# Optimization experiments

Measured on AMD Instinct MI355X. Metric: run time of the kernel, lower is better.

## Reference

```python
import jax, jax.numpy as jnp
import numpy as np

N = 262144   # collocation points (512x512 grid equivalent)
H = 64       # MLP hidden width
PI = np.float32(np.pi)


def setup_inputs() -> dict:
    key = jax.random.key(0)
    ks = jax.random.split(key, 6)
    def glorot(k, shp):
        scale = np.float32(np.sqrt(2.0 / (shp[0] + shp[1])))
        return jax.random.normal(k, shp, jnp.float32) * scale
    return {
        "points": jax.random.uniform(ks[0], (N, 2), jnp.float32),  # (x, t) in [0,1]^2
        "W1": glorot(ks[1], (2, H)), "b1": jnp.zeros((H,), jnp.float32),
        "W2": glorot(ks[2], (H, H)), "b2": jnp.zeros((H,), jnp.float32),
        "W3": glorot(ks[3], (H, H)), "b3": jnp.zeros((H,), jnp.float32),
        "Wo": glorot(ks[4], (H, 1)), "bo": jnp.zeros((1,), jnp.float32),
    }


def _mlp(pt, W1, b1, W2, b2, W3, b3, Wo, bo):
    # pt: [2] -> scalar u(x, t)
    h = jnp.tanh(pt @ W1 + b1)
    h = jnp.tanh(h @ W2 + b2)
    h = jnp.tanh(h @ W3 + b3)
    return (h @ Wo + bo)[0]


def reference(points, W1, b1, W2, b2, W3, b3, Wo, bo):
    params = (W1, b1, W2, b2, W3, b3, Wo, bo)
    dt = points.dtype
    keep_t = jnp.array([0.0, 1.0], dt)   # points * [0,1]
    set_x1 = jnp.array([1.0, 0.0], dt)   # + [1,0] -> (1, t)

    def psi_fn(pt):
        x, t = pt[0], pt[1]
        pt1t = pt * keep_t + set_x1                    # boundary point (1, t)
        u = _mlp(pt, *params)                          # u(x, t)
        u_1t = _mlp(pt1t, *params)                     # u(1, t)
        u1t_x = jax.grad(lambda p: _mlp(p, *params))(pt1t)[0]  # du/dx at (1, t)
        return (2.0 * x * jnp.sin(PI * t)
                + (t * t - t) * (x * x - x) * (u - u_1t - u1t_x))

    def loss_point(pt):
        x, t = pt[0], pt[1]
        psi, g1 = jax.value_and_grad(psi_fn)(pt)       # g1 = (psi_x, psi_t)
        # TF's tape.gradient sums over components of dpsi_dxdt, so:
        # h = grad(psi_x + psi_t) = (psi_xx + psi_tx, psi_xt + psi_tt)
        h = jax.grad(lambda p: jnp.sum(jax.grad(psi_fn)(p)))(pt)
        s = jnp.sin(PI * t)
        res = (h[0] + h[1] + psi * g1[0]
               - s * (2.0 - PI * PI * x * x + 2.0 * x ** 3 * s))
        return jnp.abs(res)

    return jnp.mean(jax.vmap(loss_point)(points))
```

## Files before the change

kernel.cpp:

```cpp
#include <hip/hip_runtime.h>
#include <math.h>

typedef _Float16 half_t;
typedef half_t half8 __attribute__((ext_vector_type(8)));
typedef __fp16 fp16x2 __attribute__((ext_vector_type(2)));
typedef float f32x4 __attribute__((ext_vector_type(4)));
typedef float f32x2 __attribute__((ext_vector_type(2)));

#define PI_F 3.14159265358979323846f

__device__ __forceinline__ f32x2 splat2(float s) { return f32x2{s, s}; }
__device__ __forceinline__ f32x2 fma2(f32x2 a, f32x2 b, f32x2 c) {
    return __builtin_elementwise_fma(a, b, c);
}

__device__ __forceinline__ f32x2 ftanh2(f32x2 z) {
    const f32x2 m = z * splat2(2.8853900817779268f);
    f32x2 t;
    t[0] = exp2f(m[0]);
    t[1] = exp2f(m[1]);
    const f32x2 s = t + splat2(1.f);
    f32x2 r;
    r[0] = __builtin_amdgcn_rcpf(s[0]);
    r[1] = __builtin_amdgcn_rcpf(s[1]);
    return fma2(splat2(-2.f), r, splat2(1.f));
}

__global__ __launch_bounds__(256) void pinn_main(
    const float* __restrict__ pts,
    const float* __restrict__ W1, const float* __restrict__ b1,
    const float* __restrict__ b2, const float* __restrict__ b3,
    const half_t* __restrict__ wsH,
    float* __restrict__ partial)
{
    __shared__ __align__(16) half_t J[160 * 64];
    __shared__ float ubuf[7][16];

    const int tid = threadIdx.x;
    const int l   = tid & 63;
    const int w   = tid >> 6;
    const int q   = l >> 4;
    const int i   = l & 15;
    const int ja  = w * 16 + i;
    const int jb  = w * 16 + q * 4;

    const int rb0 = i * 64 + ((q ^ (i & 7)) << 3);
    const int rb1 = i * 64 + (((4 + q) ^ (i & 7)) << 3);
    const int wbase = i * 64 + ((((w * 2 + (q >> 1)) ^ (i & 7))) << 3) + (q & 1) * 4;

    const half8 w2a = *(const half8*)(wsH + ja * 64 + q * 8);
    const half8 w2b = *(const half8*)(wsH + ja * 64 + 32 + q * 8);
    const half8 w3a = *(const half8*)(wsH + 4096 + ja * 64 + q * 8);
    const half8 w3b = *(const half8*)(wsH + 4096 + ja * 64 + 32 + q * 8);

    const float4 w04 = *(const float4*)(W1 + jb);
    const float4 w14 = *(const float4*)(W1 + 64 + jb);
    const float4 b14 = *(const float4*)(b1 + jb);
    const float4 b24 = *(const float4*)(b2 + jb);
    const float4 b34 = *(const float4*)(b3 + jb);

    half8 wo0 = {0, 0, 0, 0, 0, 0, 0, 0};
    half8 wo1 = {0, 0, 0, 0, 0, 0, 0, 0};
    if (i == 0) {
        wo0 = *(const half8*)(wsH + 8192 + q * 8);
        wo1 = *(const half8*)(wsH + 8192 + 32 + q * 8);
    }

    auto stc = [&](int c, f32x2 v01, f32x2 v23) {
        uint2 d;
        d.x = __builtin_bit_cast(unsigned int,
                                 __builtin_amdgcn_cvt_pkrtz(v01[0], v01[1]));
        d.y = __builtin_bit_cast(unsigned int,
                                 __builtin_amdgcn_cvt_pkrtz(v23[0], v23[1]));
        *(uint2*)(&J[wbase + c * 1024]) = d;
    };

    const f32x2 w0a = {w04.x, w04.y}, w0b = {w04.z, w04.w};
    const f32x2 w1a = {w14.x, w14.y}, w1b = {w14.z, w14.w};
    const f32x2 bba = {b14.x, b14.y}, bbb = {b14.z, b14.w};

    float bsum = 0.f;

    #pragma unroll 1
    for (int pass = 0; pass < 2; ++pass) {
        const int pbase = blockIdx.x * 32 + pass * 16;

        const float2 xy = *(const float2*)(pts + 2 * (pbase + i));
        const float X = xy.x, T = xy.y;

        {
            const f32x2 wda = w0a + w1a, wdb = w0b + w1b;
            const f32x2 zva = fma2(splat2(X), w0a, fma2(splat2(T), w1a, bba));
            const f32x2 zvb = fma2(splat2(X), w0b, fma2(splat2(T), w1b, bbb));
            const f32x2 aa = ftanh2(zva), ab = ftanh2(zvb);
            const f32x2 d1a = splat2(1.f) - aa * aa, d1b = splat2(1.f) - ab * ab;
            const f32x2 d2a = splat2(-2.f) * aa * d1a, d2b = splat2(-2.f) * ab * d1b;
            stc(0, aa, ab);
            stc(1, d1a * w0a, d1b * w0b);
            stc(2, d1a * wda, d1b * wdb);
            stc(3, d2a * wda * wda, d2b * wdb * wdb);
        }
        {
            const f32x2 zva = fma2(splat2(T), w1a, bba + w0a);
            const f32x2 zvb = fma2(splat2(T), w1b, bbb + w0b);
            const f32x2 aa = ftanh2(zva), ab = ftanh2(zvb);
            const f32x2 e1a = splat2(1.f) - aa * aa, e1b = splat2(1.f) - ab * ab;
            const f32x2 e2a = splat2(-2.f) * aa * e1a, e2b = splat2(-2.f) * ab * e1b;
            const f32x2 e3a = splat2(-2.f) * (e1a * e1a + aa * e2a);
            const f32x2 e3b = splat2(-2.f) * (e1b * e1b + ab * e2b);
            stc(4, aa, ab);
            stc(5, e1a * w0a, e1b * w0b);
            stc(6, e1a * w1a, e1b * w1b);
            stc(7, e2a * w0a * w1a, e2b * w0b * w1b);
            stc(8, e2a * w1a * w1a, e2b * w1b * w1b);
            stc(9, e3a * w0a * w1a * w1a, e3b * w0b * w1b * w1b);
        }

        auto layer_step = [&](const half8 A0, const half8 A1, const float4 b4,
                              bool combine) {
            __syncthreads();
            const f32x4 zb = {b4.x, b4.y, b4.z, b4.w};
            const f32x4 z0 = {0.f, 0.f, 0.f, 0.f};
            f32x4 acc[10];
            #pragma unroll
            for (int c = 0; c < 10; ++c) {
                const half8 f0 = *(const half8*)(&J[rb0 + c * 1024]);
                const half8 f1 = *(const half8*)(&J[rb1 + c * 1024]);
                f32x4 z = (c == 0 || c == 4) ? zb : z0;
                z = __builtin_amdgcn_mfma_f32_16x16x32_f16(A0, f0, z, 0, 0, 0);
                z = __builtin_amdgcn_mfma_f32_16x16x32_f16(A1, f1, z, 0, 0, 0);
                acc[c] = z;
            }
            __syncthreads();

            {
                const f32x2 zva = {acc[0][0], acc[0][1]}, zvb = {acc[0][2], acc[0][3]};
                const f32x2 aa = ftanh2(zva), ab = ftanh2(zvb);
                const f32x2 d1a = splat2(1.f) - aa * aa, d1b = splat2(1.f) - ab * ab;
                const f32x2 d2a = splat2(-2.f) * aa * d1a, d2b = splat2(-2.f) * ab * d1b;
                const f32x2 zxa = {acc[1][0], acc[1][1]}, zxb = {acc[1][2], acc[1][3]};
                const f32x2 zda = {acc[2][0], acc[2][1]}, zdb = {acc[2][2], acc[2][3]};
                const f32x2 zdda = {acc[3][0], acc[3][1]}, zddb = {acc[3][2], acc[3][3]};
                stc(0, aa, ab);
                stc(1, d1a * zxa, d1b * zxb);
                stc(2, d1a * zda, d1b * zdb);
                stc(3, fma2(d2a * zda, zda, d1a * zdda),
                       fma2(d2b * zdb, zdb, d1b * zddb));
            }
            {
                const f32x2 zva = {acc[4][0], acc[4][1]}, zvb = {acc[4][2], acc[4][3]};
                const f32x2 aa = ftanh2(zva), ab = ftanh2(zvb);
                const f32x2 e1a = splat2(1.f) - aa * aa, e1b = splat2(1.f) - ab * ab;
                const f32x2 e2a = splat2(-2.f) * aa * e1a, e2b = splat2(-2.f) * ab * e1b;
                const f32x2 e3a = splat2(-2.f) * (e1a * e1a + aa * e2a);
                const f32x2 e3b = splat2(-2.f) * (e1b * e1b + ab * e2b);
                const f32x2 zxa  = {acc[5][0], acc[5][1]},  zxb  = {acc[5][2], acc[5][3]};
                const f32x2 zta  = {acc[6][0], acc[6][1]},  ztb  = {acc[6][2], acc[6][3]};
                const f32x2 zxta = {acc[7][0], acc[7][1]},  zxtb = {acc[7][2], acc[7][3]};
                const f32x2 ztta = {acc[8][0], acc[8][1]},  zttb = {acc[8][2], acc[8][3]};
                const f32x2 zxtta = {acc[9][0], acc[9][1]}, zxttb = {acc[9][2], acc[9][3]};
                if (combine) {
                    stc(4, aa + e1a * zxa, ab + e1b * zxb);
                    stc(5, fma2(e2a * zxa, zta, fma2(e1a, zxta, e1a * zta)),
                           fma2(e2b * zxb, ztb, fma2(e1b, zxtb, e1b * ztb)));
                    stc(6, fma2(e2a * zta, zta,
                                fma2(e1a, ztta,
                                     fma2(e3a * zxa, zta * zta,
                                          fma2(e2a, fma2(splat2(2.f) * zxta, zta,
                                                         zxa * ztta),
                                               e1a * zxtta)))),
                           fma2(e2b * ztb, ztb,
                                fma2(e1b, zttb,
                                     fma2(e3b * zxb, ztb * ztb,
                                          fma2(e2b, fma2(splat2(2.f) * zxtb, ztb,
                                                         zxb * zttb),
                                               e1b * zxttb)))));
                } else {
                    stc(4, aa, ab);
                    stc(5, e1a * zxa, e1b * zxb);
                    stc(6, e1a * zta, e1b * ztb);
                    stc(7, fma2(e2a * zxa, zta, e1a * zxta),
                           fma2(e2b * zxb, ztb, e1b * zxtb));
                    stc(8, fma2(e2a * zta, zta, e1a * ztta),
                            fma2(e2b * ztb, ztb, e1b * zttb));
                    stc(9,
                        fma2(e3a * zxa, zta * zta,
                             fma2(e2a, fma2(splat2(2.f) * zxta, zta, zxa * ztta),
                                  e1a * zxtta)),
                        fma2(e3b * zxb, ztb * ztb,
                             fma2(e2b, fma2(splat2(2.f) * zxtb, ztb, zxb * zttb),
                                  e1b * zxttb)));
                }
            }
        };
        layer_step(w2a, w2b, b24, false);
        layer_step(w3a, w3b, b34, true);
        __syncthreads();

        {
            #pragma unroll
            for (int k3 = 0; k3 < 2; ++k3) {
                const int c = w * 2 + k3;
                if (c < 7) {
                    const half8 f0 = *(const half8*)(&J[rb0 + c * 1024]);
                    const half8 f1 = *(const half8*)(&J[rb1 + c * 1024]);
                    f32x4 z = {0.f, 0.f, 0.f, 0.f};
                    z = __builtin_amdgcn_mfma_f32_16x16x32_f16(wo0, f0, z, 0, 0, 0);
                    z = __builtin_amdgcn_mfma_f32_16x16x32_f16(wo1, f1, z, 0, 0, 0);
                    if (q == 0) ubuf[c][i] = z[0];
                }
            }
        }
        __syncthreads();

        if (tid < 16) {
            const float x = X, t = T;
            float U[7];
            #pragma unroll
            for (int c = 0; c < 7; ++c) U[c] = ubuf[c][tid];

            const float D   = U[0] - U[4];
            const float Dx  = U[1];
            const float Dd  = U[2] - U[5];
            const float Ddd = U[3] - U[6];

            const float s  = __builtin_amdgcn_sinf(0.5f * t);
            const float cc = __builtin_amdgcn_cosf(0.5f * t);
            const float A  = t * t - t,  Ap = 2.f * t - 1.f;
            const float B  = x * x - x,  Bp = 2.f * x - 1.f;

            const float psi   = 2.f * x * s + A * B * D;
            const float psi_x = 2.f * s + A * (Bp * D + B * Dx);

            const float forcing = s * (2.f - PI_F * PI_F * x * x
                                       + 2.f * x * x * x * s);
            const float res = 4.f * PI_F * cc - 2.f * PI_F * PI_F * x * s
                            + 2.f * (A + B + Ap * Bp) * D
                            + 2.f * (A * Bp + Ap * B) * Dd
                            + A * B * Ddd
                            + psi * psi_x - forcing;
            float s4 = fabsf(res);
            s4 += __shfl_xor(s4, 1, 64);
            s4 += __shfl_xor(s4, 2, 64);
            s4 += __shfl_xor(s4, 4, 64);
            s4 += __shfl_xor(s4, 8, 64);
            if (tid == 0) bsum += s4;
        }
    }

    if (tid == 0) partial[blockIdx.x] = bsum;
}

__global__ __launch_bounds__(256) void pinn_prep(
    const float* __restrict__ W2, const float* __restrict__ W3,
    const float* __restrict__ Wo, half_t* __restrict__ wsH)
{
    const int tid = threadIdx.x;
    for (int idx = tid; idx < 4096; idx += 256) {
        const int n = idx >> 6, k = idx & 63;
        wsH[idx]        = (half_t)W2[k * 64 + n];
        wsH[4096 + idx] = (half_t)W3[k * 64 + n];
    }
    if (tid < 64) wsH[8192 + tid] = (half_t)Wo[tid];
}

__global__ __launch_bounds__(256) void pinn_reduce(
    const float* __restrict__ partial, float* __restrict__ out,
    int nblocks, float invN)
{
    __shared__ float sd[256];
    float s = 0.f;
    for (int i = threadIdx.x; i < nblocks; i += 256) s += partial[i];
    sd[threadIdx.x] = s;
    __syncthreads();
    #pragma unroll
    for (int off = 128; off > 0; off >>= 1) {
        if (threadIdx.x < off) sd[threadIdx.x] += sd[threadIdx.x + off];
        __syncthreads();
    }
    if (threadIdx.x == 0) out[0] = sd[0] * invN;
}

extern "C" void kernel_launch(void* const* d_in, const int* in_sizes, int n_in,
                              void* d_out, int out_size, void* d_ws, size_t ws_size,
                              hipStream_t stream)
{
    const float* pts = (const float*)d_in[0];
    const float* W1  = (const float*)d_in[1];
    const float* b1  = (const float*)d_in[2];
    const float* W2  = (const float*)d_in[3];
    const float* b2  = (const float*)d_in[4];
    const float* W3  = (const float*)d_in[5];
    const float* b3  = (const float*)d_in[6];
    const float* Wo  = (const float*)d_in[7];

    const int nPts    = in_sizes[0] / 2;
    const int nBlocks = nPts / 32;

    half_t* wsH     = (half_t*)d_ws;
    float*  partial = (float*)((char*)d_ws + 32768);

    pinn_prep<<<1, 256, 0, stream>>>(W2, W3, Wo, wsH);
    pinn_main<<<nBlocks, 256, 0, stream>>>(pts, W1, b1, b2, b3, wsH, partial);
    pinn_reduce<<<1, 256, 0, stream>>>(partial, (float*)d_out, nBlocks,
                                       1.f / (float)nPts);
}
```

Before: 116.9 us.

## Fuse output projection into last layer epilogue via register dot and shuffles

The final Wo projection, which used to write the layer-3 tangent channels to LDS and run extra MFMAs, is now computed in fp32 straight from the layer-3 accumulators. Each lane does a dot product against its Wo slice, reduces across the quad with shuffles, and writes per-wave partials to a 4x7x16 LDS buffer that the epilogue sums. This drops one LDS write/read round trip, a barrier and a mostly idle MFMA stage. In exchange it adds shuffles and some extra VALU and register pressure, and the layer-step lambda is unrolled by hand.

```diff
diff --git a/kernel.cpp b/kernel.cpp
--- a/kernel.cpp
+++ b/kernel.cpp
@@ -30,11 +30,12 @@
     const float* __restrict__ pts,
     const float* __restrict__ W1, const float* __restrict__ b1,
     const float* __restrict__ b2, const float* __restrict__ b3,
+    const float* __restrict__ Wo,
     const half_t* __restrict__ wsH,
     float* __restrict__ partial)
 {
     __shared__ __align__(16) half_t J[160 * 64];
-    __shared__ float ubuf[7][16];
+    __shared__ float ubuf[4][7][16];
 
     const int tid = threadIdx.x;
     const int l   = tid & 63;
@@ -58,13 +59,7 @@
     const float4 b14 = *(const float4*)(b1 + jb);
     const float4 b24 = *(const float4*)(b2 + jb);
     const float4 b34 = *(const float4*)(b3 + jb);
-
-    half8 wo0 = {0, 0, 0, 0, 0, 0, 0, 0};
-    half8 wo1 = {0, 0, 0, 0, 0, 0, 0, 0};
-    if (i == 0) {
-        wo0 = *(const half8*)(wsH + 8192 + q * 8);
-        wo1 = *(const half8*)(wsH + 8192 + 32 + q * 8);
-    }
+    const float4 wo4 = *(const float4*)(Wo + jb);
 
     auto stc = [&](int c, f32x2 v01, f32x2 v23) {
         uint2 d;
@@ -78,6 +73,13 @@
     const f32x2 w0a = {w04.x, w04.y}, w0b = {w04.z, w04.w};
     const f32x2 w1a = {w14.x, w14.y}, w1b = {w14.z, w14.w};
     const f32x2 bba = {b14.x, b14.y}, bbb = {b14.z, b14.w};
+    const f32x2 woA = {wo4.x, wo4.y}, woB = {wo4.z, wo4.w};
+
+    auto dot4 = [&](f32x2 v01, f32x2 v23) -> float {
+        f32x2 t = v01 * woA;
+        t = fma2(v23, woB, t);
+        return t[0] + t[1];
+    };
 
     float bsum = 0.f;
 
@@ -116,10 +118,9 @@
             stc(9, e3a * w0a * w1a * w1a, e3b * w0b * w1b * w1b);
         }
 
-        auto layer_step = [&](const half8 A0, const half8 A1, const float4 b4,
-                              bool combine) {
+        {
             __syncthreads();
-            const f32x4 zb = {b4.x, b4.y, b4.z, b4.w};
+            const f32x4 zb = {b24.x, b24.y, b24.z, b24.w};
             const f32x4 z0 = {0.f, 0.f, 0.f, 0.f};
             f32x4 acc[10];
             #pragma unroll
@@ -127,8 +128,8 @@
                 const half8 f0 = *(const half8*)(&J[rb0 + c * 1024]);
                 const half8 f1 = *(const half8*)(&J[rb1 + c * 1024]);
                 f32x4 z = (c == 0 || c == 4) ? zb : z0;
-                z = __builtin_amdgcn_mfma_f32_16x16x32_f16(A0, f0, z, 0, 0, 0);
-                z = __builtin_amdgcn_mfma_f32_16x16x32_f16(A1, f1, z, 0, 0, 0);
+                z = __builtin_amdgcn_mfma_f32_16x16x32_f16(w2a, f0, z, 0, 0, 0);
+                z = __builtin_amdgcn_mfma_f32_16x16x32_f16(w2b, f1, z, 0, 0, 0);
                 acc[c] = z;
             }
             __syncthreads();
@@ -159,56 +160,89 @@
                 const f32x2 zxta = {acc[7][0], acc[7][1]},  zxtb = {acc[7][2], acc[7][3]};
                 const f32x2 ztta = {acc[8][0], acc[8][1]},  zttb = {acc[8][2], acc[8][3]};
                 const f32x2 zxtta = {acc[9][0], acc[9][1]}, zxttb = {acc[9][2], acc[9][3]};
-                if (combine) {
-                    stc(4, aa + e1a * zxa, ab + e1b * zxb);
-                    stc(5, fma2(e2a * zxa, zta, fma2(e1a, zxta, e1a * zta)),
-                           fma2(e2b * zxb, ztb, fma2(e1b, zxtb, e1b * ztb)));
-                    stc(6, fma2(e2a * zta, zta,
-                                fma2(e1a, ztta,
-                                     fma2(e3a * zxa, zta * zta,
-                                          fma2(e2a, fma2(splat2(2.f) * zxta, zta,
-                                                         zxa * ztta),
-                                               e1a * zxtta)))),
-                           fma2(e2b * ztb, ztb,
-                                fma2(e1b, zttb,
-                                     fma2(e3b * zxb, ztb * ztb,
-                                          fma2(e2b, fma2(splat2(2.f) * zxtb, ztb,
-                                                         zxb * zttb),
-                                               e1b * zxttb)))));
-                } else {
-                    stc(4, aa, ab);
-                    stc(5, e1a * zxa, e1b * zxb);
-                    stc(6, e1a * zta, e1b * ztb);
-                    stc(7, fma2(e2a * zxa, zta, e1a * zxta),
-                           fma2(e2b * zxb, ztb, e1b * zxtb));
-                    stc(8, fma2(e2a * zta, zta, e1a * ztta),
-                            fma2(e2b * ztb, ztb, e1b * zttb));
-                    stc(9,
-                        fma2(e3a * zxa, zta * zta,
-                             fma2(e2a, fma2(splat2(2.f) * zxta, zta, zxa * ztta),
-                                  e1a * zxtta)),
-                        fma2(e3b * zxb, ztb * ztb,
-                             fma2(e2b, fma2(splat2(2.f) * zxtb, ztb, zxb * zttb),
-                                  e1b * zxttb)));
-                }
-            }
-        };
-        layer_step(w2a, w2b, b24, false);
-        layer_step(w3a, w3b, b34, true);
-        __syncthreads();
+                stc(4, aa, ab);
+                stc(5, e1a * zxa, e1b * zxb);
+                stc(6, e1a * zta, e1b * ztb);
+                stc(7, fma2(e2a * zxa, zta, e1a * zxta),
+                       fma2(e2b * zxb, ztb, e1b * zxtb));
+                stc(8, fma2(e2a * zta, zta, e1a * ztta),
+                        fma2(e2b * ztb, ztb, e1b * zttb));
+                stc(9,
+                    fma2(e3a * zxa, zta * zta,
+                         fma2(e2a, fma2(splat2(2.f) * zxta, zta, zxa * ztta),
+                              e1a * zxtta)),
+                    fma2(e3b * zxb, ztb * ztb,
+                         fma2(e2b, fma2(splat2(2.f) * zxtb, ztb, zxb * zttb),
+                              e1b * zxttb)));
+            }
+        }
 
         {
+            __syncthreads();
+            const f32x4 zb = {b34.x, b34.y, b34.z, b34.w};
+            const f32x4 z0 = {0.f, 0.f, 0.f, 0.f};
+            f32x4 acc[10];
             #pragma unroll
-            for (int k3 = 0; k3 < 2; ++k3) {
-                const int c = w * 2 + k3;
-                if (c < 7) {
-                    const half8 f0 = *(const half8*)(&J[rb0 + c * 1024]);
-                    const half8 f1 = *(const half8*)(&J[rb1 + c * 1024]);
-                    f32x4 z = {0.f, 0.f, 0.f, 0.f};
-                    z = __builtin_amdgcn_mfma_f32_16x16x32_f16(wo0, f0, z, 0, 0, 0);
-                    z = __builtin_amdgcn_mfma_f32_16x16x32_f16(wo1, f1, z, 0, 0, 0);
-                    if (q == 0) ubuf[c][i] = z[0];
-                }
+            for (int c = 0; c < 10; ++c) {
+                const half8 f0 = *(const half8*)(&J[rb0 + c * 1024]);
+                const half8 f1 = *(const half8*)(&J[rb1 + c * 1024]);
+                f32x4 z = (c == 0 || c == 4) ? zb : z0;
+                z = __builtin_amdgcn_mfma_f32_16x16x32_f16(w3a, f0, z, 0, 0, 0);
+                z = __builtin_amdgcn_mfma_f32_16x16x32_f16(w3b, f1, z, 0, 0, 0);
+                acc[c] = z;
+            }
+
+            float s[7];
+            {
+                const f32x2 zva = {acc[0][0], acc[0][1]}, zvb = {acc[0][2], acc[0][3]};
+                const f32x2 aa = ftanh2(zva), ab = ftanh2(zvb);
+                const f32x2 d1a = splat2(1.f) - aa * aa, d1b = splat2(1.f) - ab * ab;
+                const f32x2 d2a = splat2(-2.f) * aa * d1a, d2b = splat2(-2.f) * ab * d1b;
+                const f32x2 zxa = {acc[1][0], acc[1][1]}, zxb = {acc[1][2], acc[1][3]};
+                const f32x2 zda = {acc[2][0], acc[2][1]}, zdb = {acc[2][2], acc[2][3]};
+                const f32x2 zdda = {acc[3][0], acc[3][1]}, zddb = {acc[3][2], acc[3][3]};
+                s[0] = dot4(aa, ab);
+                s[1] = dot4(d1a * zxa, d1b * zxb);
+                s[2] = dot4(d1a * zda, d1b * zdb);
+                s[3] = dot4(fma2(d2a * zda, zda, d1a * zdda),
+                            fma2(d2b * zdb, zdb, d1b * zddb));
+            }
+            {
+                const f32x2 zva = {acc[4][0], acc[4][1]}, zvb = {acc[4][2], acc[4][3]};
+                const f32x2 aa = ftanh2(zva), ab = ftanh2(zvb);
+                const f32x2 e1a = splat2(1.f) - aa * aa, e1b = splat2(1.f) - ab * ab;
+                const f32x2 e2a = splat2(-2.f) * aa * e1a, e2b = splat2(-2.f) * ab * e1b;
+                const f32x2 e3a = splat2(-2.f) * (e1a * e1a + aa * e2a);
+                const f32x2 e3b = splat2(-2.f) * (e1b * e1b + ab * e2b);
+                const f32x2 zxa  = {acc[5][0], acc[5][1]},  zxb  = {acc[5][2], acc[5][3]};
+                const f32x2 zta  = {acc[6][0], acc[6][1]},  ztb  = {acc[6][2], acc[6][3]};
+                const f32x2 zxta = {acc[7][0], acc[7][1]},  zxtb = {acc[7][2], acc[7][3]};
+                const f32x2 ztta = {acc[8][0], acc[8][1]},  zttb = {acc[8][2], acc[8][3]};
+                const f32x2 zxtta = {acc[9][0], acc[9][1]}, zxttb = {acc[9][2], acc[9][3]};
+                s[4] = dot4(aa + e1a * zxa, ab + e1b * zxb);
+                s[5] = dot4(fma2(e2a * zxa, zta, fma2(e1a, zxta, e1a * zta)),
+                            fma2(e2b * zxb, ztb, fma2(e1b, zxtb, e1b * ztb)));
+                s[6] = dot4(fma2(e2a * zta, zta,
+                                 fma2(e1a, ztta,
+                                      fma2(e3a * zxa, zta * zta,
+                                           fma2(e2a, fma2(splat2(2.f) * zxta, zta,
+                                                          zxa * ztta),
+                                                e1a * zxtta)))),
+                            fma2(e2b * ztb, ztb,
+                                 fma2(e1b, zttb,
+                                      fma2(e3b * zxb, ztb * ztb,
+                                           fma2(e2b, fma2(splat2(2.f) * zxtb, ztb,
+                                                          zxb * zttb),
+                                                e1b * zxttb)))));
+            }
+            #pragma unroll
+            for (int c = 0; c < 7; ++c) {
+                s[c] += __shfl_xor(s[c], 16, 64);
+                s[c] += __shfl_xor(s[c], 32, 64);
+            }
+            if (l < 16) {
+                #pragma unroll
+                for (int c = 0; c < 7; ++c) ubuf[w][c][l] = s[c];
             }
         }
         __syncthreads();
@@ -217,7 +251,9 @@
             const float x = X, t = T;
             float U[7];
             #pragma unroll
-            for (int c = 0; c < 7; ++c) U[c] = ubuf[c][tid];
+            for (int c = 0; c < 7; ++c)
+                U[c] = (ubuf[0][c][tid] + ubuf[1][c][tid])
+                     + (ubuf[2][c][tid] + ubuf[3][c][tid]);
 
             const float D   = U[0] - U[4];
             const float Dx  = U[1];
@@ -253,7 +289,7 @@
 
 __global__ __launch_bounds__(256) void pinn_prep(
     const float* __restrict__ W2, const float* __restrict__ W3,
-    const float* __restrict__ Wo, half_t* __restrict__ wsH)
+    half_t* __restrict__ wsH)
 {
     const int tid = threadIdx.x;
     for (int idx = tid; idx < 4096; idx += 256) {
@@ -261,7 +297,6 @@
         wsH[idx]        = (half_t)W2[k * 64 + n];
         wsH[4096 + idx] = (half_t)W3[k * 64 + n];
     }
-    if (tid < 64) wsH[8192 + tid] = (half_t)Wo[tid];
 }
 
 __global__ __launch_bounds__(256) void pinn_reduce(
@@ -300,8 +335,8 @@
     half_t* wsH     = (half_t*)d_ws;
     float*  partial = (float*)((char*)d_ws + 32768);
 
-    pinn_prep<<<1, 256, 0, stream>>>(W2, W3, Wo, wsH);
-    pinn_main<<<nBlocks, 256, 0, stream>>>(pts, W1, b1, b2, b3, wsH, partial);
+    pinn_prep<<<1, 256, 0, stream>>>(W2, W3, wsH);
+    pinn_main<<<nBlocks, 256, 0, stream>>>(pts, W1, b1, b2, b3, Wo, wsH, partial);
     pinn_reduce<<<1, 256, 0, stream>>>(partial, (float*)d_out, nBlocks,
                                        1.f / (float)nPts);
 }
```

Result: slower. 122.9 us (+5.2%).
